# Kernel optimization log

Measured on AMD Instinct MI355X. Metric: run time of the kernel, lower is better.

Reference implementation:

```python
import jax, jax.numpy as jnp
import numpy as np

HEADS = 8
EPS = 1e-6
LN_EPS = 1e-5


def avg_pool(x, k):
    b, c, h, w = x.shape
    return x.reshape(b, c, h // k, k, w // k, k).mean(axis=(3, 5))


def layernorm(x, g, b):
    mu = x.mean(-1, keepdims=True)
    var = x.var(-1, keepdims=True)
    return (x - mu) / jnp.sqrt(var + LN_EPS) * g + b


def pos_embed_2d(h, w, c):
    # original calls build_2d_sincos_position_embedding(w=h, h=w): grid over (h, w), row-major flatten
    gw, gh = jnp.meshgrid(jnp.arange(h, dtype=jnp.float32),
                          jnp.arange(w, dtype=jnp.float32), indexing='ij')
    pd = c // 4
    omega = 1.0 / (10000.0 ** (jnp.arange(pd, dtype=jnp.float32) / pd))
    ow = gw.reshape(-1, 1) * omega  # (h*w, pd)
    oh = gh.reshape(-1, 1) * omega
    return jnp.concatenate([jnp.sin(ow), jnp.cos(ow), jnp.sin(oh), jnp.cos(oh)], axis=1)  # (h*w, c)


def _forward(a3, a4, q_w, q_b, q_ln_g, q_ln_b, k_w, k_b, k_ln_g, k_ln_b,
             v_w, v_b, out_w, out_b, lin1_w, lin1_b, lin2_w, lin2_b,
             n1_g, n1_b, n2_g, n2_b, idx):
    orig_a3 = a3
    if idx == 2:
        a3d = avg_pool(a3, 2)
    else:
        a3d = avg_pool(a3, 4)
        a4 = avg_pool(a4, 2)
    bs, c, h, w = a3d.shape
    L = h * w  # tgt_len == src_len (a3_down and a4 have equal spatial size)
    hd = c // HEADS

    residual = a3d.reshape(bs, c, L).transpose(0, 2, 1)  # (b, L, c)
    x3 = residual
    x4 = a4.reshape(bs, c, L).transpose(0, 2, 1)
    pos = pos_embed_2d(h, w, c)  # (L, c)
    x3 = x3 + pos[None]
    x4 = x4 + pos[None]

    Q = layernorm(x3 @ q_w + q_b, q_ln_g, q_ln_b)
    K = layernorm(x4 @ k_w + k_b, k_ln_g, k_ln_b)
    V = x4 @ v_w + v_b
    Q = jax.nn.relu(Q).reshape(bs, L, HEADS, hd).transpose(0, 2, 1, 3)  # (b,h,L,d)
    K = jax.nn.relu(K).reshape(bs, L, HEADS, hd).transpose(0, 2, 1, 3)
    V = V.reshape(bs, L, HEADS, hd).transpose(0, 2, 1, 3)

    # cosFormer position reweighting: index = pi/2 * (1..m) / m
    m = L
    wi = (np.pi / 2.0) * jnp.arange(1, m + 1, dtype=jnp.float32) / m  # (m,)
    sn = jnp.sin(wi)[None, None, :, None]
    cs = jnp.cos(wi)[None, None, :, None]
    Q_ = jnp.concatenate([Q * sn, Q * cs], axis=-1)  # (b,h,L,2d)
    K_ = jnp.concatenate([K * sn, K * cs], axis=-1)

    KV = jnp.einsum('bhld,bhlm->bhdm', K_, V)                     # (b,h,2d,d)
    Z = 1.0 / jnp.maximum(jnp.einsum('bhld,bhd->bhl', Q_, K_.sum(axis=2)), EPS)
    attn = jnp.einsum('bhld,bhdm->bhlm', Q_, KV) * Z[..., None]   # (b,h,L,d)
    attn = attn.transpose(0, 2, 1, 3).reshape(bs, L, c)

    out = attn @ out_w + out_b
    out = layernorm(out, n1_g, n1_b)     # normalize_before=False -> norm1 applied
    out = residual + out                 # dropout=0
    res2 = out
    out = jax.nn.gelu(out @ lin1_w + lin1_b, approximate=False) @ lin2_w + lin2_b
    out = layernorm(out, n2_g, n2_b)
    out = res2 + out

    a3sa = out.transpose(0, 2, 1).reshape(bs, c, h, w)
    a3sa = jax.image.resize(a3sa, orig_a3.shape, method='bilinear')  # align_corners=False
    return a3sa * orig_a3


def setup_inputs() -> dict:
    key = jax.random.key(0)
    ks = jax.random.split(key, 10)
    B, C = 16, 256
    C4 = 4 * C

    def w(k, shp):
        return jax.random.normal(k, shp, dtype=jnp.float32) * 0.02

    return {
        'a3': jax.random.normal(ks[0], (B, C, 128, 128), dtype=jnp.float32),
        'a4': jax.random.normal(ks[1], (B, C, 64, 64), dtype=jnp.float32),
        'q_w': w(ks[2], (C, C)), 'q_b': jnp.zeros((C,), jnp.float32),
        'q_ln_g': jnp.ones((C,), jnp.float32), 'q_ln_b': jnp.zeros((C,), jnp.float32),
        'k_w': w(ks[3], (C, C)), 'k_b': jnp.zeros((C,), jnp.float32),
        'k_ln_g': jnp.ones((C,), jnp.float32), 'k_ln_b': jnp.zeros((C,), jnp.float32),
        'v_w': w(ks[4], (C, C)), 'v_b': jnp.zeros((C,), jnp.float32),
        'out_w': w(ks[5], (C, C)), 'out_b': jnp.zeros((C,), jnp.float32),
        'lin1_w': w(ks[6], (C, C4)), 'lin1_b': jnp.zeros((C4,), jnp.float32),
        'lin2_w': w(ks[7], (C4, C)), 'lin2_b': jnp.zeros((C,), jnp.float32),
        'n1_g': jnp.ones((C,), jnp.float32), 'n1_b': jnp.zeros((C,), jnp.float32),
        'n2_g': jnp.ones((C,), jnp.float32), 'n2_b': jnp.zeros((C,), jnp.float32),
        'idx': 2,
    }


def reference(a3, a4, q_w, q_b, q_ln_g, q_ln_b, k_w, k_b, k_ln_g, k_ln_b,
              v_w, v_b, out_w, out_b, lin1_w, lin1_b, lin2_w, lin2_b,
              n1_g, n1_b, n2_g, n2_b, idx):
    return _forward(a3, a4, q_w, q_b, q_ln_g, q_ln_b, k_w, k_b, k_ln_g, k_ln_b,
                    v_w, v_b, out_w, out_b, lin1_w, lin1_b, lin2_w, lin2_b,
                    n1_g, n1_b, n2_g, n2_b, idx)
```

## Files before the change

### kernel.cpp

```cpp
#include <hip/hip_runtime.h>
#include <hip/hip_bf16.h>
#include <math.h>

#define HEADS 8
#define LL 4096
#define CDIM 256
#define BATCH 16
#define NROWS (BATCH*LL)

typedef __attribute__((ext_vector_type(8))) __bf16 bf16x8;
typedef __attribute__((ext_vector_type(4))) __bf16 bf16x4;
typedef __attribute__((ext_vector_type(4))) float f32x4;

__device__ inline float b2f(ushort u) {
    union { unsigned u; float f; } v; v.u = ((unsigned)u) << 16; return v.f;
}
__device__ inline ushort f2b(float f) {
    union { float f; unsigned u; } v; v.f = f;
    unsigned r = (v.u + 0x7FFF + ((v.u >> 16) & 1)) >> 16;
    return (ushort)r;
}
__device__ inline void gload16(const void* g, void* l) {
    __builtin_amdgcn_global_load_lds(
        (const __attribute__((address_space(1))) unsigned int*)g,
        (__attribute__((address_space(3))) unsigned int*)l, 16, 0, 0);
}
__device__ inline float fast_gelu(float v) {
    float u = 0.7978845608028654f * v * (1.0f + 0.044715f * v * v);
    float e = exp2f(u * 2.885390081777927f);
    float t = 1.0f - 2.0f / (e + 1.0f);
    return 0.5f * v * (1.0f + t);
}

__global__ __launch_bounds__(256) void prep_kernel(
    float* __restrict__ pos, float* __restrict__ snc,
    const float* __restrict__ q_w, const float* __restrict__ k_w,
    const float* __restrict__ v_w, const float* __restrict__ o_w,
    const float* __restrict__ w1, const float* __restrict__ w2,
    ushort* __restrict__ wqT, ushort* __restrict__ wkT,
    ushort* __restrict__ wvT, ushort* __restrict__ woT,
    ushort* __restrict__ w1T, ushort* __restrict__ w2T,
    float* __restrict__ ksglob)
{
    __shared__ float t[32][33];
    int bid = blockIdx.x;
    int tid = threadIdx.x;
    if (bid == 1792) {
        for (int i = tid; i < BATCH * 2 * 256; i += 256) ksglob[i] = 0.0f;
        return;
    }
    if (bid < 1024) {
        int c = tid;
        int k = c & 63;
        float omega = expf(-(float)k * (9.210340371976184f / 64.0f));
        #pragma unroll
        for (int i = 0; i < 4; ++i) {
            int l = bid * 4 + i;
            int y = l >> 6, x = l & 63;
            float coord = (c < 128) ? (float)y : (float)x;
            float ang = coord * omega;
            float val = ((c & 127) < 64) ? sinf(ang) : cosf(ang);
            pos[l * CDIM + c] = val;
            if (c < 2) {
                float wi = 1.5707963267948966f * (float)(l + 1) / (float)LL;
                snc[l * 2 + c] = (c == 0) ? sinf(wi) : cosf(wi);
            }
        }
        return;
    }
    int id = bid - 1024;
    const float* W; ushort* Wt; int K, N, kb, nb;
    if (id < 64)       { W = q_w; Wt = wqT; K = 256;  N = 256;  kb = (id & 7) * 32;  nb = (id >> 3) * 32; }
    else if (id < 128) { id -= 64;  W = k_w; Wt = wkT; K = 256;  N = 256;  kb = (id & 7) * 32;  nb = (id >> 3) * 32; }
    else if (id < 192) { id -= 128; W = v_w; Wt = wvT; K = 256;  N = 256;  kb = (id & 7) * 32;  nb = (id >> 3) * 32; }
    else if (id < 256) { id -= 192; W = o_w; Wt = woT; K = 256;  N = 256;  kb = (id & 7) * 32;  nb = (id >> 3) * 32; }
    else if (id < 512) { id -= 256; W = w1;  Wt = w1T; K = 256;  N = 1024; kb = (id & 7) * 32;  nb = (id >> 3) * 32; }
    else               { id -= 512; W = w2;  Wt = w2T; K = 1024; N = 256;  kb = (id & 31) * 32; nb = (id >> 5) * 32; }
    int x = tid & 31, y = tid >> 5;
    #pragma unroll
    for (int i = 0; i < 4; ++i)
        t[y + i * 8][x] = W[(size_t)(kb + y + i * 8) * N + nb + x];
    __syncthreads();
    #pragma unroll
    for (int i = 0; i < 4; ++i) {
        int n = y + i * 8;
        Wt[(size_t)(nb + n) * K + kb + x] = f2b(t[x][n]);
    }
}

__global__ __launch_bounds__(256) void pool_x3_kernel(
    const float* __restrict__ a3, ushort* __restrict__ residual,
    ushort* __restrict__ x3b, const float* __restrict__ pos)
{
    __shared__ float raw[64][128];
    __shared__ float pooled[64][65];
    int i = blockIdx.x, ct = blockIdx.y, b = blockIdx.z;
    int tid = threadIdx.x;
    #pragma unroll
    for (int it = 0; it < 8; ++it) {
        int lin = (it * 256 + tid) * 4;
        int x = lin & 127;
        int cc = lin >> 7;
        size_t base = ((size_t)(b * 256 + ct * 64 + cc) * 128 + 2 * i) * 128 + x;
        float4 v0 = *(const float4*)&a3[base];
        float4 v1 = *(const float4*)&a3[base + 128];
        float4 s = make_float4(v0.x + v1.x, v0.y + v1.y, v0.z + v1.z, v0.w + v1.w);
        *(float4*)&raw[cc][x] = s;
    }
    __syncthreads();
    #pragma unroll
    for (int it = 0; it < 16; ++it) {
        int idx = it * 256 + tid;
        int j = idx & 63, cc = idx >> 6;
        pooled[cc][j] = 0.25f * (raw[cc][2 * j] + raw[cc][2 * j + 1]);
    }
    __syncthreads();
    #pragma unroll
    for (int it = 0; it < 16; ++it) {
        int cc = tid & 63;
        int jj = (tid >> 6) + it * 4;
        float val = pooled[cc][jj];
        int l = i * 64 + jj;
        int c = ct * 64 + cc;
        size_t o = (size_t)(b * LL + l) * CDIM + c;
        residual[o] = f2b(val);
        x3b[o] = f2b(val + pos[l * CDIM + c]);
    }
}

__global__ __launch_bounds__(256) void x4_kernel(
    const float* __restrict__ a4, ushort* __restrict__ x4b, const float* __restrict__ pos)
{
    __shared__ float t2[64][65];
    int y = blockIdx.x, ct = blockIdx.y, b = blockIdx.z, tid = threadIdx.x;
    #pragma unroll
    for (int it = 0; it < 16; ++it) {
        int idx = it * 256 + tid;
        int x = idx & 63, cc = idx >> 6;
        t2[cc][x] = a4[((size_t)(b * 256 + ct * 64 + cc) * 64 + y) * 64 + x];
    }
    __syncthreads();
    #pragma unroll
    for (int it = 0; it < 16; ++it) {
        int cc = tid & 63;
        int xx = (tid >> 6) + it * 4;
        int l = y * 64 + xx, c = ct * 64 + cc;
        x4b[(size_t)(b * LL + l) * CDIM + c] = f2b(t2[cc][xx] + pos[l * CDIM + c]);
    }
}

template<bool DO_LN, bool DO_RELU, bool DO_RES>
__global__ __launch_bounds__(512, 4) void gemm_mfma(
    const ushort* __restrict__ A, const ushort* __restrict__ Wt,
    const float* __restrict__ bias, const float* __restrict__ gam_,
    const float* __restrict__ bet_, const ushort* __restrict__ res,
    ushort* __restrict__ outb)
{
    __shared__ ushort As[2][128 * 32];
    __shared__ ushort Bs[2][256 * 32];
    __shared__ float redS[128][4];
    __shared__ float redQ[128][4];
    __shared__ float2 mustd[128];

    const int tid = threadIdx.x;
    const int lane = tid & 63;
    const int wv = tid >> 6;
    const int wr = wv >> 2;
    const int wc = wv & 3;
    const int wvu = __builtin_amdgcn_readfirstlane(wv);
    const int row0 = blockIdx.x * 128;

    const int sr = tid >> 2;
    const int sg = (tid & 3) ^ ((sr >> 1) & 3);
    const ushort* aSrc = A + (size_t)(row0 + sr) * 256 + sg * 8;
    const ushort* bSrc0 = Wt + (size_t)sr * 256 + sg * 8;
    const ushort* bSrc1 = Wt + (size_t)(128 + sr) * 256 + sg * 8;

    const int frSlot = (lane >> 4) ^ (((lane & 15) >> 1) & 3);

    f32x4 acc[4][4] = {};
    gload16(aSrc, (char*)&As[0][0] + wvu * 1024);
    gload16(bSrc0, (char*)&Bs[0][0] + wvu * 1024);
    gload16(bSrc1, (char*)&Bs[0][0] + 8192 + wvu * 1024);
    __syncthreads();

    int cur = 0;
    for (int t = 0; t < 8; ++t) {
        if (t < 7) {
            gload16(aSrc + (t + 1) * 32, (char*)&As[cur ^ 1][0] + wvu * 1024);
            gload16(bSrc0 + (t + 1) * 32, (char*)&Bs[cur ^ 1][0] + wvu * 1024);
            gload16(bSrc1 + (t + 1) * 32, (char*)&Bs[cur ^ 1][0] + 8192 + wvu * 1024);
        }
        bf16x8 af[4], bfr[4];
        #pragma unroll
        for (int f = 0; f < 4; ++f) {
            int r = wr * 64 + f * 16 + (lane & 15);
            af[f] = *(const bf16x8*)&As[cur][r * 32 + frSlot * 8];
            int c = wc * 64 + f * 16 + (lane & 15);
            bfr[f] = *(const bf16x8*)&Bs[cur][c * 32 + frSlot * 8];
        }
        #pragma unroll
        for (int fi = 0; fi < 4; ++fi)
            #pragma unroll
            for (int fj = 0; fj < 4; ++fj)
                acc[fi][fj] = __builtin_amdgcn_mfma_f32_16x16x32_bf16(
                    af[fi], bfr[fj], acc[fi][fj], 0, 0, 0);
        __syncthreads();
        cur ^= 1;
    }

    const int cl = lane & 15;
    const int rg = lane >> 4;
    float bia[4], gmv[4], btv[4];
    #pragma unroll
    for (int fj = 0; fj < 4; ++fj) {
        int col = wc * 64 + fj * 16 + cl;
        bia[fj] = bias[col];
        if constexpr (DO_LN) { gmv[fj] = gam_[col]; btv[fj] = bet_[col]; }
    }
    #pragma unroll
    for (int fi = 0; fi < 4; ++fi)
        #pragma unroll
        for (int fj = 0; fj < 4; ++fj)
            #pragma unroll
            for (int j = 0; j < 4; ++j)
                acc[fi][fj][j] += bia[fj];

    if constexpr (DO_LN) {
        #pragma unroll
        for (int fi = 0; fi < 4; ++fi)
            #pragma unroll
            for (int j = 0; j < 4; ++j) {
                float s = acc[fi][0][j] + acc[fi][1][j] + acc[fi][2][j] + acc[fi][3][j];
                float q = acc[fi][0][j] * acc[fi][0][j] + acc[fi][1][j] * acc[fi][1][j]
                        + acc[fi][2][j] * acc[fi][2][j] + acc[fi][3][j] * acc[fi][3][j];
                #pragma unroll
                for (int m = 1; m <= 8; m <<= 1) {
                    s += __shfl_xor(s, m, 64);
                    q += __shfl_xor(q, m, 64);
                }
                if (cl == 0) {
                    int tr = wr * 64 + fi * 16 + rg * 4 + j;
                    redS[tr][wc] = s; redQ[tr][wc] = q;
                }
            }
        __syncthreads();
        if (tid < 128) {
            float s = redS[tid][0] + redS[tid][1] + redS[tid][2] + redS[tid][3];
            float q = redQ[tid][0] + redQ[tid][1] + redQ[tid][2] + redQ[tid][3];
            float mu = s * (1.0f / 256.0f);
            float var = q * (1.0f / 256.0f) - mu * mu;
            mustd[tid] = make_float2(mu, rsqrtf(var + 1e-5f));
        }
        __syncthreads();
        #pragma unroll
        for (int fi = 0; fi < 4; ++fi)
            #pragma unroll
            for (int j = 0; j < 4; ++j) {
                float2 ms = mustd[wr * 64 + fi * 16 + rg * 4 + j];
                #pragma unroll
                for (int fj = 0; fj < 4; ++fj)
                    acc[fi][fj][j] = (acc[fi][fj][j] - ms.x) * ms.y * gmv[fj] + btv[fj];
            }
    }
    if constexpr (DO_RELU) {
        #pragma unroll
        for (int fi = 0; fi < 4; ++fi)
            #pragma unroll
            for (int fj = 0; fj < 4; ++fj)
                #pragma unroll
                for (int j = 0; j < 4; ++j)
                    acc[fi][fj][j] = fmaxf(acc[fi][fj][j], 0.0f);
    }
    #pragma unroll
    for (int fi = 0; fi < 4; ++fi)
        #pragma unroll
        for (int j = 0; j < 4; ++j) {
            size_t row = row0 + wr * 64 + fi * 16 + rg * 4 + j;
            size_t rbase = row * 256 + wc * 64 + cl;
            #pragma unroll
            for (int fj = 0; fj < 4; ++fj) {
                float v = acc[fi][fj][j];
                if constexpr (DO_RES) v += b2f(res[rbase + fj * 16]);
                outb[rbase + fj * 16] = f2b(v);
            }
        }
}

__global__ __launch_bounds__(512, 2) void gemm_kv(
    const ushort* __restrict__ A, const ushort* __restrict__ wkT,
    const ushort* __restrict__ wvT, const float* __restrict__ k_b,
    const float* __restrict__ k_g, const float* __restrict__ k_beta,
    const float* __restrict__ v_b, const float* __restrict__ snc,
    float* __restrict__ ksglob, ushort* __restrict__ Kb, ushort* __restrict__ Vb)
{
    __shared__ ushort As[2][128 * 32];
    __shared__ ushort BsK[2][256 * 32];
    __shared__ ushort BsV[2][256 * 32];
    __shared__ float redS[128][4];
    __shared__ float redQ[128][4];
    __shared__ float2 mustd[128];

    const int tid = threadIdx.x;
    const int lane = tid & 63;
    const int wv = tid >> 6;
    const int wr = wv >> 2;
    const int wc = wv & 3;
    const int wvu = __builtin_amdgcn_readfirstlane(wv);
    const int row0 = blockIdx.x * 128;

    const int sr = tid >> 2;
    const int sg = (tid & 3) ^ ((sr >> 1) & 3);
    const ushort* aSrc = A + (size_t)(row0 + sr) * 256 + sg * 8;
    const ushort* bkSrc0 = wkT + (size_t)sr * 256 + sg * 8;
    const ushort* bkSrc1 = wkT + (size_t)(128 + sr) * 256 + sg * 8;
    const ushort* bvSrc0 = wvT + (size_t)sr * 256 + sg * 8;
    const ushort* bvSrc1 = wvT + (size_t)(128 + sr) * 256 + sg * 8;

    const int frSlot = (lane >> 4) ^ (((lane & 15) >> 1) & 3);

    f32x4 accK[4][4] = {};
    f32x4 accV[4][4] = {};
    gload16(aSrc, (char*)&As[0][0] + wvu * 1024);
    gload16(bkSrc0, (char*)&BsK[0][0] + wvu * 1024);
    gload16(bkSrc1, (char*)&BsK[0][0] + 8192 + wvu * 1024);
    gload16(bvSrc0, (char*)&BsV[0][0] + wvu * 1024);
    gload16(bvSrc1, (char*)&BsV[0][0] + 8192 + wvu * 1024);
    __syncthreads();

    int cur = 0;
    for (int t = 0; t < 8; ++t) {
        if (t < 7) {
            gload16(aSrc + (t + 1) * 32, (char*)&As[cur ^ 1][0] + wvu * 1024);
            gload16(bkSrc0 + (t + 1) * 32, (char*)&BsK[cur ^ 1][0] + wvu * 1024);
            gload16(bkSrc1 + (t + 1) * 32, (char*)&BsK[cur ^ 1][0] + 8192 + wvu * 1024);
            gload16(bvSrc0 + (t + 1) * 32, (char*)&BsV[cur ^ 1][0] + wvu * 1024);
            gload16(bvSrc1 + (t + 1) * 32, (char*)&BsV[cur ^ 1][0] + 8192 + wvu * 1024);
        }
        bf16x8 af[4], bk[4], bv[4];
        #pragma unroll
        for (int f = 0; f < 4; ++f) {
            int r = wr * 64 + f * 16 + (lane & 15);
            af[f] = *(const bf16x8*)&As[cur][r * 32 + frSlot * 8];
            int c = wc * 64 + f * 16 + (lane & 15);
            bk[f] = *(const bf16x8*)&BsK[cur][c * 32 + frSlot * 8];
            bv[f] = *(const bf16x8*)&BsV[cur][c * 32 + frSlot * 8];
        }
        #pragma unroll
        for (int fi = 0; fi < 4; ++fi)
            #pragma unroll
            for (int fj = 0; fj < 4; ++fj) {
                accK[fi][fj] = __builtin_amdgcn_mfma_f32_16x16x32_bf16(
                    af[fi], bk[fj], accK[fi][fj], 0, 0, 0);
                accV[fi][fj] = __builtin_amdgcn_mfma_f32_16x16x32_bf16(
                    af[fi], bv[fj], accV[fi][fj], 0, 0, 0);
            }
        __syncthreads();
        cur ^= 1;
    }

    const int cl = lane & 15;
    const int rg = lane >> 4;
    #pragma unroll
    for (int fj = 0; fj < 4; ++fj) {
        float bv_ = v_b[wc * 64 + fj * 16 + cl];
        #pragma unroll
        for (int fi = 0; fi < 4; ++fi)
            #pragma unroll
            for (int j = 0; j < 4; ++j)
                accV[fi][fj][j] += bv_;
    }
    #pragma unroll
    for (int fi = 0; fi < 4; ++fi)
        #pragma unroll
        for (int j = 0; j < 4; ++j) {
            size_t rbase = (size_t)(row0 + wr * 64 + fi * 16 + rg * 4 + j) * 256 + wc * 64 + cl;
            #pragma unroll
            for (int fj = 0; fj < 4; ++fj)
                Vb[rbase + fj * 16] = f2b(accV[fi][fj][j]);
        }
    float bia[4], gmv[4], btv[4];
    #pragma unroll
    for (int fj = 0; fj < 4; ++fj) {
        int col = wc * 64 + fj * 16 + cl;
        bia[fj] = k_b[col]; gmv[fj] = k_g[col]; btv[fj] = k_beta[col];
    }
    #pragma unroll
    for (int fi = 0; fi < 4; ++fi)
        #pragma unroll
        for (int fj = 0; fj < 4; ++fj)
            #pragma unroll
            for (int j = 0; j < 4; ++j)
                accK[fi][fj][j] += bia[fj];
    #pragma unroll
    for (int fi = 0; fi < 4; ++fi)
        #pragma unroll
        for (int j = 0; j < 4; ++j) {
            float s = accK[fi][0][j] + accK[fi][1][j] + accK[fi][2][j] + accK[fi][3][j];
            float q = accK[fi][0][j] * accK[fi][0][j] + accK[fi][1][j] * accK[fi][1][j]
                    + accK[fi][2][j] * accK[fi][2][j] + accK[fi][3][j] * accK[fi][3][j];
            #pragma unroll
            for (int m = 1; m <= 8; m <<= 1) {
                s += __shfl_xor(s, m, 64);
                q += __shfl_xor(q, m, 64);
            }
            if (cl == 0) {
                int tr = wr * 64 + fi * 16 + rg * 4 + j;
                redS[tr][wc] = s; redQ[tr][wc] = q;
            }
        }
    __syncthreads();
    if (tid < 128) {
        float s = redS[tid][0] + redS[tid][1] + redS[tid][2] + redS[tid][3];
        float q = redQ[tid][0] + redQ[tid][1] + redQ[tid][2] + redQ[tid][3];
        float mu = s * (1.0f / 256.0f);
        float var = q * (1.0f / 256.0f) - mu * mu;
        mustd[tid] = make_float2(mu, rsqrtf(var + 1e-5f));
    }
    __syncthreads();
    float kss[4] = {}, ksc[4] = {};
    #pragma unroll
    for (int fi = 0; fi < 4; ++fi)
        #pragma unroll
        for (int j = 0; j < 4; ++j) {
            int rloc = wr * 64 + fi * 16 + rg * 4 + j;
            float2 ms = mustd[rloc];
            int l = (row0 + rloc) & (LL - 1);
            float sn = snc[l * 2], cs = snc[l * 2 + 1];
            size_t rbase = (size_t)(row0 + rloc) * 256 + wc * 64 + cl;
            #pragma unroll
            for (int fj = 0; fj < 4; ++fj) {
                float v = (accK[fi][fj][j] - ms.x) * ms.y * gmv[fj] + btv[fj];
                v = fmaxf(v, 0.0f);
                Kb[rbase + fj * 16] = f2b(v);
                kss[fj] += sn * v;
                ksc[fj] += cs * v;
            }
        }
    int b = row0 >> 12;
    #pragma unroll
    for (int fj = 0; fj < 4; ++fj) {
        float s = kss[fj], c = ksc[fj];
        s += __shfl_xor(s, 16, 64); s += __shfl_xor(s, 32, 64);
        c += __shfl_xor(c, 16, 64); c += __shfl_xor(c, 32, 64);
        if (rg == 0) {
            int col = wc * 64 + fj * 16 + cl;
            atomicAdd(&ksglob[((size_t)b * 2 + 0) * 256 + col], s);
            atomicAdd(&ksglob[((size_t)b * 2 + 1) * 256 + col], c);
        }
    }
}

__global__ __launch_bounds__(256, 2) void mlp_fused(
    const ushort* __restrict__ res2, const ushort* __restrict__ w1T,
    const ushort* __restrict__ w2T, const float* __restrict__ b1,
    const float* __restrict__ b2, const float* __restrict__ gam_,
    const float* __restrict__ bet_, ushort* __restrict__ outb)
{
    __shared__ ushort As[2][64 * 32];
    __shared__ ushort Bs[2][256 * 32];
    __shared__ ushort h1c[8 * 64 * 36];
    __shared__ float redS[64][4];
    __shared__ float redQ[64][4];
    __shared__ float2 mustd[64];

    const int tid = threadIdx.x;
    const int lane = tid & 63;
    const int wv = tid >> 6;
    const int wvu = __builtin_amdgcn_readfirstlane(wv);
    const int row0 = blockIdx.x * 64;
    const int sr = tid >> 2;
    const int sg = (tid & 3) ^ ((sr >> 1) & 3);
    const ushort* aSrc = res2 + (size_t)(row0 + sr) * 256 + sg * 8;
    const int frSlot = (lane >> 4) ^ (((lane & 15) >> 1) & 3);
    const int cl = lane & 15;
    const int rg = lane >> 4;

    f32x4 acc2[4][4] = {};
    gload16(aSrc, (char*)&As[0][0] + wvu * 1024);
    #pragma unroll
    for (int j = 0; j < 4; ++j)
        gload16(w1T + (size_t)(j * 64 + sr) * 256 + sg * 8,
                (char*)&Bs[0][0] + j * 4096 + wvu * 1024);
    __syncthreads();
    int cur = 0;

    for (int c = 0; c < 4; ++c) {
        const ushort* b1Src = w1T + (size_t)(c * 256 + sr) * 256 + sg * 8;
        const ushort* b2Src = w2T + (size_t)sr * 1024 + c * 256 + sg * 8;
        f32x4 acc1[4][4] = {};
        for (int t = 0; t < 8; ++t) {
            if (t < 7) {
                gload16(aSrc + (t + 1) * 32, (char*)&As[cur ^ 1][0] + wvu * 1024);
                #pragma unroll
                for (int j = 0; j < 4; ++j)
                    gload16(b1Src + j * 64 * 256 + (t + 1) * 32,
                            (char*)&Bs[cur ^ 1][0] + j * 4096 + wvu * 1024);
            } else {
                gload16(aSrc, (char*)&As[cur ^ 1][0] + wvu * 1024);
                #pragma unroll
                for (int j = 0; j < 4; ++j)
                    gload16(b2Src + (size_t)j * 64 * 1024,
                            (char*)&Bs[cur ^ 1][0] + j * 4096 + wvu * 1024);
            }
            bf16x8 af[4], bfr[4];
            #pragma unroll
            for (int f = 0; f < 4; ++f) {
                int r = f * 16 + (lane & 15);
                af[f] = *(const bf16x8*)&As[cur][r * 32 + frSlot * 8];
                int cc2 = wv * 64 + f * 16 + (lane & 15);
                bfr[f] = *(const bf16x8*)&Bs[cur][cc2 * 32 + frSlot * 8];
            }
            #pragma unroll
            for (int fi = 0; fi < 4; ++fi)
                #pragma unroll
                for (int fj = 0; fj < 4; ++fj)
                    acc1[fi][fj] = __builtin_amdgcn_mfma_f32_16x16x32_bf16(
                        af[fi], bfr[fj], acc1[fi][fj], 0, 0, 0);
            __syncthreads();
            cur ^= 1;
        }
        float bia1[4];
        #pragma unroll
        for (int fj = 0; fj < 4; ++fj)
            bia1[fj] = b1[c * 256 + wv * 64 + fj * 16 + cl];
        #pragma unroll
        for (int fi = 0; fi < 4; ++fi)
            #pragma unroll
            for (int fj = 0; fj < 4; ++fj) {
                int tch = wv * 2 + (fj >> 1);
                int kk_local = (fj & 1) * 16 + cl;
                #pragma unroll
                for (int j = 0; j < 4; ++j) {
                    float v = acc1[fi][fj][j] + bia1[fj];
                    float g = fast_gelu(v);
                    int row = fi * 16 + rg * 4 + j;
                    h1c[tch * 2304 + row * 36 + kk_local] = f2b(g);
                }
            }
        __syncthreads();
        for (int t = 0; t < 8; ++t) {
            if (t < 7) {
                #pragma unroll
                for (int j = 0; j < 4; ++j)
                    gload16(b2Src + (size_t)j * 64 * 1024 + (t + 1) * 32,
                            (char*)&Bs[cur ^ 1][0] + j * 4096 + wvu * 1024);
            } else {
                int cn = (c < 3) ? c + 1 : 3;
                #pragma unroll
                for (int j = 0; j < 4; ++j)
                    gload16(w1T + (size_t)(cn * 256 + j * 64 + sr) * 256 + sg * 8,
                            (char*)&Bs[cur ^ 1][0] + j * 4096 + wvu * 1024);
            }
            bf16x8 af[4], bfr[4];
            #pragma unroll
            for (int f = 0; f < 4; ++f) {
                int r = f * 16 + (lane & 15);
                int ho = t * 2304 + r * 36 + (lane >> 4) * 8;
                bf16x4 lo = *(const bf16x4*)&h1c[ho];
                bf16x4 hi = *(const bf16x4*)&h1c[ho + 4];
                bf16x8 a_;
                a_[0] = lo[0]; a_[1] = lo[1]; a_[2] = lo[2]; a_[3] = lo[3];
                a_[4] = hi[0]; a_[5] = hi[1]; a_[6] = hi[2]; a_[7] = hi[3];
                af[f] = a_;
                int cc2 = wv * 64 + f * 16 + (lane & 15);
                bfr[f] = *(const bf16x8*)&Bs[cur][cc2 * 32 + frSlot * 8];
            }
            #pragma unroll
            for (int fi = 0; fi < 4; ++fi)
                #pragma unroll
                for (int fj = 0; fj < 4; ++fj)
                    acc2[fi][fj] = __builtin_amdgcn_mfma_f32_16x16x32_bf16(
                        af[fi], bfr[fj], acc2[fi][fj], 0, 0, 0);
            __syncthreads();
            cur ^= 1;
        }
    }
    float bia[4], gmv[4], btv[4];
    #pragma unroll
    for (int fj = 0; fj < 4; ++fj) {
        int col = wv * 64 + fj * 16 + cl;
        bia[fj] = b2[col];
        gmv[fj] = gam_[col];
        btv[fj] = bet_[col];
    }
    #pragma unroll
    for (int fi = 0; fi < 4; ++fi)
        #pragma unroll
        for (int fj = 0; fj < 4; ++fj)
            #pragma unroll
            for (int j = 0; j < 4; ++j)
                acc2[fi][fj][j] += bia[fj];
    #pragma unroll
    for (int fi = 0; fi < 4; ++fi)
        #pragma unroll
        for (int j = 0; j < 4; ++j) {
            float s = acc2[fi][0][j] + acc2[fi][1][j] + acc2[fi][2][j] + acc2[fi][3][j];
            float q = acc2[fi][0][j] * acc2[fi][0][j] + acc2[fi][1][j] * acc2[fi][1][j]
                    + acc2[fi][2][j] * acc2[fi][2][j] + acc2[fi][3][j] * acc2[fi][3][j];
            #pragma unroll
            for (int m = 1; m <= 8; m <<= 1) {
                s += __shfl_xor(s, m, 64);
                q += __shfl_xor(q, m, 64);
            }
            if (cl == 0) { redS[fi * 16 + rg * 4 + j][wv] = s; redQ[fi * 16 + rg * 4 + j][wv] = q; }
        }
    __syncthreads();
    if (tid < 64) {
        float s = redS[tid][0] + redS[tid][1] + redS[tid][2] + redS[tid][3];
        float q = redQ[tid][0] + redQ[tid][1] + redQ[tid][2] + redQ[tid][3];
        float mu = s * (1.0f / 256.0f);
        float var = q * (1.0f / 256.0f) - mu * mu;
        mustd[tid] = make_float2(mu, rsqrtf(var + 1e-5f));
    }
    __syncthreads();
    #pragma unroll
    for (int fi = 0; fi < 4; ++fi)
        #pragma unroll
        for (int j = 0; j < 4; ++j) {
            float2 ms = mustd[fi * 16 + rg * 4 + j];
            size_t row = row0 + fi * 16 + rg * 4 + j;
            size_t rbase = row * 256 + wv * 64 + cl;
            #pragma unroll
            for (int fj = 0; fj < 4; ++fj) {
                float v = (acc2[fi][fj][j] - ms.x) * ms.y * gmv[fj] + btv[fj];
                v += b2f(res2[rbase + fj * 16]);
                outb[rbase + fj * 16] = f2b(v);
            }
        }
}

__global__ __launch_bounds__(256) void kv_kernel(
    const ushort* __restrict__ Kmat, const ushort* __restrict__ Vmat,
    const float* __restrict__ snc, float* __restrict__ kvpart)
{
    __shared__ float Kt[64][36];
    __shared__ float Vt[64][36];
    __shared__ float sns[64], css[64];
    int chunk = blockIdx.x;
    int bh = blockIdx.y;
    int b = bh >> 3, h = bh & 7;
    int tid = threadIdx.x;
    int m = tid & 31;
    int d0 = (tid >> 5) * 4;
    float accs[4] = {}, accc[4] = {};
    int l0chunk = chunk * 512;
    int lrow = tid >> 2;
    int lcol = (tid & 3) * 8;
    for (int sub = 0; sub < 8; ++sub) {
        int l0 = l0chunk + sub * 64;
        {
            size_t gbase = (size_t)(b * LL + l0 + lrow) * CDIM + h * 32 + lcol;
            uint4 kr = *(const uint4*)&Kmat[gbase];
            uint4 vr = *(const uint4*)&Vmat[gbase];
            float* kd = &Kt[lrow][lcol];
            float* vd = &Vt[lrow][lcol];
            kd[0] = b2f((ushort)(kr.x & 0xffff)); kd[1] = b2f((ushort)(kr.x >> 16));
            kd[2] = b2f((ushort)(kr.y & 0xffff)); kd[3] = b2f((ushort)(kr.y >> 16));
            kd[4] = b2f((ushort)(kr.z & 0xffff)); kd[5] = b2f((ushort)(kr.z >> 16));
            kd[6] = b2f((ushort)(kr.w & 0xffff)); kd[7] = b2f((ushort)(kr.w >> 16));
            vd[0] = b2f((ushort)(vr.x & 0xffff)); vd[1] = b2f((ushort)(vr.x >> 16));
            vd[2] = b2f((ushort)(vr.y & 0xffff)); vd[3] = b2f((ushort)(vr.y >> 16));
            vd[4] = b2f((ushort)(vr.z & 0xffff)); vd[5] = b2f((ushort)(vr.z >> 16));
            vd[6] = b2f((ushort)(vr.w & 0xffff)); vd[7] = b2f((ushort)(vr.w >> 16));
        }
        if (tid < 64) { sns[tid] = snc[(l0 + tid) * 2]; css[tid] = snc[(l0 + tid) * 2 + 1]; }
        __syncthreads();
        #pragma unroll 4
        for (int lt = 0; lt < 64; ++lt) {
            float v = Vt[lt][m];
            float vs = v * sns[lt];
            float vc = v * css[lt];
            float4 kd4 = *(const float4*)&Kt[lt][d0];
            accs[0] += kd4.x * vs; accc[0] += kd4.x * vc;
            accs[1] += kd4.y * vs; accc[1] += kd4.y * vc;
            accs[2] += kd4.z * vs; accc[2] += kd4.z * vc;
            accs[3] += kd4.w * vs; accc[3] += kd4.w * vc;
        }
        __syncthreads();
    }
    size_t base = (size_t)(bh * 8 + chunk) * 2048;
    #pragma unroll
    for (int i2 = 0; i2 < 4; ++i2) {
        kvpart[base + (d0 + i2) * 32 + m] = accs[i2];
        kvpart[base + 1024 + (d0 + i2) * 32 + m] = accc[i2];
    }
}

__global__ __launch_bounds__(256) void kvred_kernel(
    const float* __restrict__ kvpart, const float* __restrict__ ksglob,
    ushort* __restrict__ Bimg)
{
    int bh = blockIdx.x;
    int b = bh >> 3, h = bh & 7;
    int tid = threadIdx.x;
    for (int e = tid; e < 2560; e += 256) {
        int n = e >> 5;
        int k = e & 31;
        int t = n >> 4, col = n & 15;
        float v = 0.0f;
        if (t < 4) {
            int off = (t >= 2 ? 1024 : 0) + k * 32 + (t & 1) * 16 + col;
            #pragma unroll
            for (int ch = 0; ch < 8; ++ch)
                v += kvpart[(size_t)(bh * 8 + ch) * 2048 + off];
        } else if (col < 2) {
            v = ksglob[((size_t)b * 2 + col) * 256 + h * 32 + k];
        }
        ushort hi = f2b(v);
        ushort lo = f2b(v - b2f(hi));
        Bimg[(size_t)bh * 5120 + n * 32 + k] = hi;
        Bimg[(size_t)bh * 5120 + (80 + n) * 32 + k] = lo;
    }
}

__global__ __launch_bounds__(256, 2) void attn_mfma(
    const ushort* __restrict__ Qmat, const ushort* __restrict__ Bimg,
    const float* __restrict__ snc, ushort* __restrict__ attnOut)
{
    __shared__ ushort Bs[5120];
    int ltile = blockIdx.x, h = blockIdx.y, b = blockIdx.z;
    int bh = b * 8 + h;
    int tid = threadIdx.x;
    int lane = tid & 63;
    int wv = tid >> 6;

    for (int e = tid; e < 640; e += 256)
        *(uint4*)&Bs[e * 8] = *(const uint4*)&Bimg[(size_t)bh * 5120 + e * 8];
    __syncthreads();

    bf16x8 bfr[10];
    #pragma unroll
    for (int tt = 0; tt < 10; ++tt) {
        int row = (tt < 5 ? tt * 16 : 80 + (tt - 5) * 16) + (lane & 15);
        bfr[tt] = *(const bf16x8*)&Bs[row * 32 + (lane >> 4) * 8];
    }
    int lbase = ltile * 256 + wv * 64;
    bf16x8 af[4];
    #pragma unroll
    for (int fi = 0; fi < 4; ++fi) {
        int l = lbase + fi * 16 + (lane & 15);
        af[fi] = *(const bf16x8*)&Qmat[(size_t)(b * LL + l) * CDIM + h * 32 + (lane >> 4) * 8];
    }
    f32x4 acc[4][5] = {};
    #pragma unroll
    for (int fi = 0; fi < 4; ++fi)
        #pragma unroll
        for (int t = 0; t < 5; ++t) {
            acc[fi][t] = __builtin_amdgcn_mfma_f32_16x16x32_bf16(af[fi], bfr[t], acc[fi][t], 0, 0, 0);
            acc[fi][t] = __builtin_amdgcn_mfma_f32_16x16x32_bf16(af[fi], bfr[t + 5], acc[fi][t], 0, 0, 0);
        }

    int zlane = lane & 48;
    int cl = lane & 15;
    #pragma unroll
    for (int fi = 0; fi < 4; ++fi) {
        #pragma unroll
        for (int j = 0; j < 4; ++j) {
            float zraw = acc[fi][4][j];
            float zs = __shfl(zraw, zlane, 64);
            float zc = __shfl(zraw, zlane | 1, 64);
            int l = lbase + fi * 16 + ((lane >> 4) & 3) * 4 + j;
            float sn = snc[l * 2], cs = snc[l * 2 + 1];
            float den = sn * zs + cs * zc;
            float Z = 1.0f / fmaxf(den, 1e-6f);
            float v0 = (sn * acc[fi][0][j] + cs * acc[fi][2][j]) * Z;
            float v1 = (sn * acc[fi][1][j] + cs * acc[fi][3][j]) * Z;
            size_t ob = (size_t)(b * LL + l) * CDIM + h * 32 + cl;
            attnOut[ob] = f2b(v0);
            attnOut[ob + 16] = f2b(v1);
        }
    }
}

__global__ __launch_bounds__(256) void resize_mul_kernel(
    const ushort* __restrict__ ffeat, const float* __restrict__ a3, float* __restrict__ out)
{
    __shared__ float ft[3][64][65];
    int k = blockIdx.x, ct = blockIdx.y, b = blockIdx.z;
    int tid = threadIdx.x;
    for (int it = 0; it < 48; ++it) {
        int e = it * 256 + tid;
        int cc = e & 63;
        int xs = (e >> 6) & 63;
        int ys = e >> 12;
        int ysrc = min(max(k - 1 + ys, 0), 63);
        ft[ys][cc][xs] = b2f(ffeat[(size_t)(b * LL + ysrc * 64 + xs) * CDIM + ct * 64 + cc]);
    }
    __syncthreads();
    int x = tid & 127;
    int half = tid >> 7;
    int y = 2 * k + half;
    int ysA, ysB; float wyA, wyB;
    if (half == 0) { ysA = 0; ysB = 1; wyA = 0.25f; wyB = 0.75f; }
    else           { ysA = 1; ysB = 2; wyA = 0.75f; wyB = 0.25f; }
    int x0; float wx1;
    if ((x & 1) == 0) { x0 = x / 2 - 1; wx1 = 0.75f; }
    else              { x0 = x / 2;     wx1 = 0.25f; }
    int x0c = max(x0, 0);
    int x1c = min(x0 + 1, 63);
    float wx0 = 1.0f - wx1;
    for (int cc = 0; cc < 64; ++cc) {
        float rA = wx0 * ft[ysA][cc][x0c] + wx1 * ft[ysA][cc][x1c];
        float rB = wx0 * ft[ysB][cc][x0c] + wx1 * ft[ysB][cc][x1c];
        float val = wyA * rA + wyB * rB;
        size_t oidx = ((size_t)(b * 256 + ct * 64 + cc) * 128 + y) * 128 + x;
        out[oidx] = val * a3[oidx];
    }
}

extern "C" void kernel_launch(void* const* d_in, const int* in_sizes, int n_in,
                              void* d_out, int out_size, void* d_ws, size_t ws_size,
                              hipStream_t stream)
{
    const float* a3     = (const float*)d_in[0];
    const float* a4     = (const float*)d_in[1];
    const float* q_w    = (const float*)d_in[2];
    const float* q_b    = (const float*)d_in[3];
    const float* q_ln_g = (const float*)d_in[4];
    const float* q_ln_b = (const float*)d_in[5];
    const float* k_w    = (const float*)d_in[6];
    const float* k_b    = (const float*)d_in[7];
    const float* k_ln_g = (const float*)d_in[8];
    const float* k_ln_b = (const float*)d_in[9];
    const float* v_w    = (const float*)d_in[10];
    const float* v_b    = (const float*)d_in[11];
    const float* out_w  = (const float*)d_in[12];
    const float* out_b  = (const float*)d_in[13];
    const float* lin1_w = (const float*)d_in[14];
    const float* lin1_b = (const float*)d_in[15];
    const float* lin2_w = (const float*)d_in[16];
    const float* lin2_b = (const float*)d_in[17];
    const float* n1_g   = (const float*)d_in[18];
    const float* n1_b   = (const float*)d_in[19];
    const float* n2_g   = (const float*)d_in[20];
    const float* n2_b   = (const float*)d_in[21];
    float* out = (float*)d_out;
    char* base = (char*)d_ws;

    const size_t MiB = 1024 * 1024;
    float*  pos      = (float*)(base);
    float*  snc      = (float*)(base + 4 * MiB);
    ushort* wqT      = (ushort*)(base + 4 * MiB + 64 * 1024);
    ushort* wkT      = wqT + 256 * 256;
    ushort* wvT      = wkT + 256 * 256;
    ushort* woT      = wvT + 256 * 256;
    ushort* w1T      = woT + 256 * 256;
    ushort* w2T      = w1T + 1024 * 256;
    ushort* residual = (ushort*)(base + 6 * MiB);
    ushort* x3b      = (ushort*)(base + 38 * MiB);
    ushort* x4b      = (ushort*)(base + 70 * MiB);
    ushort* Qb       = (ushort*)(base + 102 * MiB);
    ushort* Kb       = (ushort*)(base + 134 * MiB);
    ushort* Vb       = (ushort*)(base + 166 * MiB);
    float*  kvp      = (float*)(base + 198 * MiB);
    float*  ksglob   = (float*)(base + 206 * MiB);
    ushort* Bimg     = (ushort*)(base + 207 * MiB);
    ushort* attnb    = x3b;
    ushort* res2b    = x4b;
    ushort* ffeat    = residual;

    prep_kernel<<<1793, 256, 0, stream>>>(pos, snc, q_w, k_w, v_w, out_w, lin1_w, lin2_w,
                                          wqT, wkT, wvT, woT, w1T, w2T, ksglob);
    pool_x3_kernel<<<dim3(64, 4, 16), 256, 0, stream>>>(a3, residual, x3b, pos);
    x4_kernel<<<dim3(64, 4, 16), 256, 0, stream>>>(a4, x4b, pos);

    gemm_mfma<true, true, false><<<NROWS / 128, 512, 0, stream>>>(
        x3b, wqT, q_b, q_ln_g, q_ln_b, nullptr, Qb);
    gemm_kv<<<NROWS / 128, 512, 0, stream>>>(
        x4b, wkT, wvT, k_b, k_ln_g, k_ln_b, v_b, snc, ksglob, Kb, Vb);

    kv_kernel<<<dim3(8, 128), 256, 0, stream>>>(Kb, Vb, snc, kvp);
    kvred_kernel<<<128, 256, 0, stream>>>(kvp, ksglob, Bimg);
    attn_mfma<<<dim3(16, 8, 16), 256, 0, stream>>>(Qb, Bimg, snc, attnb);

    gemm_mfma<true, false, true><<<NROWS / 128, 512, 0, stream>>>(
        attnb, woT, out_b, n1_g, n1_b, residual, res2b);
    mlp_fused<<<NROWS / 64, 256, 0, stream>>>(
        res2b, w1T, w2T, lin1_b, lin2_b, n2_g, n2_b, ffeat);

    resize_mul_kernel<<<dim3(64, 4, 16), 256, 0, stream>>>(ffeat, a3, out);
}
```

Before: 549.6 us.

## Merge pooling kernels, raise MFMA wave priority, vectorize resize feature loads

```diff
diff --git a/kernel.cpp b/kernel.cpp
--- a/kernel.cpp
+++ b/kernel.cpp
@@ -88,64 +88,63 @@
     }
 }
 
-__global__ __launch_bounds__(256) void pool_x3_kernel(
-    const float* __restrict__ a3, ushort* __restrict__ residual,
-    ushort* __restrict__ x3b, const float* __restrict__ pos)
+__global__ __launch_bounds__(256) void pool_x4_kernel(
+    const float* __restrict__ a3, const float* __restrict__ a4,
+    ushort* __restrict__ residual, ushort* __restrict__ x3b,
+    ushort* __restrict__ x4b, const float* __restrict__ pos)
 {
     __shared__ float raw[64][128];
     __shared__ float pooled[64][65];
-    int i = blockIdx.x, ct = blockIdx.y, b = blockIdx.z;
     int tid = threadIdx.x;
-    #pragma unroll
-    for (int it = 0; it < 8; ++it) {
-        int lin = (it * 256 + tid) * 4;
-        int x = lin & 127;
-        int cc = lin >> 7;
-        size_t base = ((size_t)(b * 256 + ct * 64 + cc) * 128 + 2 * i) * 128 + x;
-        float4 v0 = *(const float4*)&a3[base];
-        float4 v1 = *(const float4*)&a3[base + 128];
-        float4 s = make_float4(v0.x + v1.x, v0.y + v1.y, v0.z + v1.z, v0.w + v1.w);
-        *(float4*)&raw[cc][x] = s;
-    }
-    __syncthreads();
-    #pragma unroll
-    for (int it = 0; it < 16; ++it) {
-        int idx = it * 256 + tid;
-        int j = idx & 63, cc = idx >> 6;
-        pooled[cc][j] = 0.25f * (raw[cc][2 * j] + raw[cc][2 * j + 1]);
-    }
-    __syncthreads();
-    #pragma unroll
-    for (int it = 0; it < 16; ++it) {
-        int cc = tid & 63;
-        int jj = (tid >> 6) + it * 4;
-        float val = pooled[cc][jj];
-        int l = i * 64 + jj;
-        int c = ct * 64 + cc;
-        size_t o = (size_t)(b * LL + l) * CDIM + c;
-        residual[o] = f2b(val);
-        x3b[o] = f2b(val + pos[l * CDIM + c]);
-    }
-}
-
-__global__ __launch_bounds__(256) void x4_kernel(
-    const float* __restrict__ a4, ushort* __restrict__ x4b, const float* __restrict__ pos)
-{
-    __shared__ float t2[64][65];
-    int y = blockIdx.x, ct = blockIdx.y, b = blockIdx.z, tid = threadIdx.x;
-    #pragma unroll
-    for (int it = 0; it < 16; ++it) {
-        int idx = it * 256 + tid;
-        int x = idx & 63, cc = idx >> 6;
-        t2[cc][x] = a4[((size_t)(b * 256 + ct * 64 + cc) * 64 + y) * 64 + x];
-    }
-    __syncthreads();
-    #pragma unroll
-    for (int it = 0; it < 16; ++it) {
-        int cc = tid & 63;
-        int xx = (tid >> 6) + it * 4;
-        int l = y * 64 + xx, c = ct * 64 + cc;
-        x4b[(size_t)(b * LL + l) * CDIM + c] = f2b(t2[cc][xx] + pos[l * CDIM + c]);
+    int ct = blockIdx.y;
+    if (blockIdx.z < 16) {
+        int i = blockIdx.x, b = blockIdx.z;
+        #pragma unroll
+        for (int it = 0; it < 8; ++it) {
+            int lin = (it * 256 + tid) * 4;
+            int x = lin & 127;
+            int cc = lin >> 7;
+            size_t base = ((size_t)(b * 256 + ct * 64 + cc) * 128 + 2 * i) * 128 + x;
+            float4 v0 = *(const float4*)&a3[base];
+            float4 v1 = *(const float4*)&a3[base + 128];
+            float4 s = make_float4(v0.x + v1.x, v0.y + v1.y, v0.z + v1.z, v0.w + v1.w);
+            *(float4*)&raw[cc][x] = s;
+        }
+        __syncthreads();
+        #pragma unroll
+        for (int it = 0; it < 16; ++it) {
+            int idx = it * 256 + tid;
+            int j = idx & 63, cc = idx >> 6;
+            pooled[cc][j] = 0.25f * (raw[cc][2 * j] + raw[cc][2 * j + 1]);
+        }
+        __syncthreads();
+        #pragma unroll
+        for (int it = 0; it < 16; ++it) {
+            int cc = tid & 63;
+            int jj = (tid >> 6) + it * 4;
+            float val = pooled[cc][jj];
+            int l = i * 64 + jj;
+            int c = ct * 64 + cc;
+            size_t o = (size_t)(b * LL + l) * CDIM + c;
+            residual[o] = f2b(val);
+            x3b[o] = f2b(val + pos[l * CDIM + c]);
+        }
+    } else {
+        int y = blockIdx.x, b = blockIdx.z - 16;
+        #pragma unroll
+        for (int it = 0; it < 16; ++it) {
+            int idx = it * 256 + tid;
+            int x = idx & 63, cc = idx >> 6;
+            pooled[cc][x] = a4[((size_t)(b * 256 + ct * 64 + cc) * 64 + y) * 64 + x];
+        }
+        __syncthreads();
+        #pragma unroll
+        for (int it = 0; it < 16; ++it) {
+            int cc = tid & 63;
+            int xx = (tid >> 6) + it * 4;
+            int l = y * 64 + xx, c = ct * 64 + cc;
+            x4b[(size_t)(b * LL + l) * CDIM + c] = f2b(pooled[cc][xx] + pos[l * CDIM + c]);
+        }
     }
 }
 
@@ -199,12 +198,14 @@
             int c = wc * 64 + f * 16 + (lane & 15);
             bfr[f] = *(const bf16x8*)&Bs[cur][c * 32 + frSlot * 8];
         }
+        __builtin_amdgcn_s_setprio(1);
         #pragma unroll
         for (int fi = 0; fi < 4; ++fi)
             #pragma unroll
             for (int fj = 0; fj < 4; ++fj)
                 acc[fi][fj] = __builtin_amdgcn_mfma_f32_16x16x32_bf16(
                     af[fi], bfr[fj], acc[fi][fj], 0, 0, 0);
+        __builtin_amdgcn_s_setprio(0);
         __syncthreads();
         cur ^= 1;
     }
@@ -346,6 +347,7 @@
             bk[f] = *(const bf16x8*)&BsK[cur][c * 32 + frSlot * 8];
             bv[f] = *(const bf16x8*)&BsV[cur][c * 32 + frSlot * 8];
         }
+        __builtin_amdgcn_s_setprio(1);
         #pragma unroll
         for (int fi = 0; fi < 4; ++fi)
             #pragma unroll
@@ -355,6 +357,7 @@
                 accV[fi][fj] = __builtin_amdgcn_mfma_f32_16x16x32_bf16(
                     af[fi], bv[fj], accV[fi][fj], 0, 0, 0);
             }
+        __builtin_amdgcn_s_setprio(0);
         __syncthreads();
         cur ^= 1;
     }
@@ -511,12 +514,14 @@
                 int cc2 = wv * 64 + f * 16 + (lane & 15);
                 bfr[f] = *(const bf16x8*)&Bs[cur][cc2 * 32 + frSlot * 8];
             }
+            __builtin_amdgcn_s_setprio(1);
             #pragma unroll
             for (int fi = 0; fi < 4; ++fi)
                 #pragma unroll
                 for (int fj = 0; fj < 4; ++fj)
                     acc1[fi][fj] = __builtin_amdgcn_mfma_f32_16x16x32_bf16(
                         af[fi], bfr[fj], acc1[fi][fj], 0, 0, 0);
+            __builtin_amdgcn_s_setprio(0);
             __syncthreads();
             cur ^= 1;
         }
@@ -566,12 +571,14 @@
                 int cc2 = wv * 64 + f * 16 + (lane & 15);
                 bfr[f] = *(const bf16x8*)&Bs[cur][cc2 * 32 + frSlot * 8];
             }
+            __builtin_amdgcn_s_setprio(1);
             #pragma unroll
             for (int fi = 0; fi < 4; ++fi)
                 #pragma unroll
                 for (int fj = 0; fj < 4; ++fj)
                     acc2[fi][fj] = __builtin_amdgcn_mfma_f32_16x16x32_bf16(
                         af[fi], bfr[fj], acc2[fi][fj], 0, 0, 0);
+            __builtin_amdgcn_s_setprio(0);
             __syncthreads();
             cur ^= 1;
         }
@@ -743,6 +750,7 @@
         af[fi] = *(const bf16x8*)&Qmat[(size_t)(b * LL + l) * CDIM + h * 32 + (lane >> 4) * 8];
     }
     f32x4 acc[4][5] = {};
+    __builtin_amdgcn_s_setprio(1);
     #pragma unroll
     for (int fi = 0; fi < 4; ++fi)
         #pragma unroll
@@ -750,6 +758,7 @@
             acc[fi][t] = __builtin_amdgcn_mfma_f32_16x16x32_bf16(af[fi], bfr[t], acc[fi][t], 0, 0, 0);
             acc[fi][t] = __builtin_amdgcn_mfma_f32_16x16x32_bf16(af[fi], bfr[t + 5], acc[fi][t], 0, 0, 0);
         }
+    __builtin_amdgcn_s_setprio(0);
 
     int zlane = lane & 48;
     int cl = lane & 15;
@@ -779,13 +788,19 @@
     __shared__ float ft[3][64][65];
     int k = blockIdx.x, ct = blockIdx.y, b = blockIdx.z;
     int tid = threadIdx.x;
-    for (int it = 0; it < 48; ++it) {
+    #pragma unroll
+    for (int it = 0; it < 6; ++it) {
         int e = it * 256 + tid;
-        int cc = e & 63;
-        int xs = (e >> 6) & 63;
-        int ys = e >> 12;
+        int cg = e & 7;
+        int xs = (e >> 3) & 63;
+        int ys = e >> 9;
         int ysrc = min(max(k - 1 + ys, 0), 63);
-        ft[ys][cc][xs] = b2f(ffeat[(size_t)(b * LL + ysrc * 64 + xs) * CDIM + ct * 64 + cc]);
+        uint4 raw = *(const uint4*)&ffeat[(size_t)(b * LL + ysrc * 64 + xs) * CDIM + ct * 64 + cg * 8];
+        float* dst = &ft[ys][cg * 8][xs];
+        dst[0]   = b2f((ushort)(raw.x & 0xffff)); dst[65]  = b2f((ushort)(raw.x >> 16));
+        dst[130] = b2f((ushort)(raw.y & 0xffff)); dst[195] = b2f((ushort)(raw.y >> 16));
+        dst[260] = b2f((ushort)(raw.z & 0xffff)); dst[325] = b2f((ushort)(raw.z >> 16));
+        dst[390] = b2f((ushort)(raw.w & 0xffff)); dst[455] = b2f((ushort)(raw.w >> 16));
     }
     __syncthreads();
     int x = tid & 127;
@@ -862,8 +877,7 @@
 
     prep_kernel<<<1793, 256, 0, stream>>>(pos, snc, q_w, k_w, v_w, out_w, lin1_w, lin2_w,
                                           wqT, wkT, wvT, woT, w1T, w2T, ksglob);
-    pool_x3_kernel<<<dim3(64, 4, 16), 256, 0, stream>>>(a3, residual, x3b, pos);
-    x4_kernel<<<dim3(64, 4, 16), 256, 0, stream>>>(a4, x4b, pos);
+    pool_x4_kernel<<<dim3(64, 4, 32), 256, 0, stream>>>(a3, a4, residual, x3b, x4b, pos);
 
     gemm_mfma<true, true, false><<<NROWS / 128, 512, 0, stream>>>(
         x3b, wqT, q_b, q_ln_g, q_ln_b, nullptr, Qb);
```

Result: faster. 528.9 us (-3.8%).
